# Kernel tuning notes

Hardware: AMD Instinct MI355X
Metric: run time of the kernel (lower is better)

The kernel has to match this reference:

```python
import jax, jax.numpy as jnp
import numpy as np

B, P, C = 128, 8732, 21          # batch, num_priors (SSD300), num_classes incl. background
TOP_K = 200
VAR0, VAR1 = 0.1, 0.2            # SSD prior variances
CONF_THRESH = 0.01
NMS_THRESH = 0.45


def setup_inputs() -> dict:
    key = jax.random.key(0)
    k1, k2, k3, k4 = jax.random.split(key, 4)
    loc_data = jax.random.normal(k1, (B, P, 4), jnp.float32)
    conf_data = jax.random.normal(k2, (B * P, C), jnp.float32)
    # priors: (cx, cy, w, h) in [0,1], positive widths/heights
    cxy = jax.random.uniform(k3, (P, 2), jnp.float32)
    wh = jax.random.uniform(k4, (P, 2), jnp.float32, minval=0.02, maxval=0.3)
    prior_data = jnp.concatenate([cxy, wh], axis=-1)
    return {"loc_data": loc_data, "conf_data": conf_data, "prior_data": prior_data}


def _decode(loc, priors):
    # loc: [B,P,4], priors: [P,4] (cx,cy,w,h) -> corner boxes [B,P,4]
    xy = priors[:, :2] + loc[..., :2] * VAR0 * priors[:, 2:]
    wh = priors[:, 2:] * jnp.exp(loc[..., 2:] * VAR1)
    return jnp.concatenate([xy - wh * 0.5, xy + wh * 0.5], axis=-1)


def _nms_single(boxes, scores, idxs):
    # boxes [P,4] corners, scores [P] (-1 where below conf_thresh), idxs [P] int class ids
    x1, y1, x2, y2 = boxes[:, 0], boxes[:, 1], boxes[:, 2], boxes[:, 3]
    areas = (x2 - x1) * (y2 - y1)

    def body(s, _):
        i = jnp.argmax(s)          # highest remaining score
        si = s[i]
        valid = si > 0.0
        bi = boxes[i]
        # IoU of bi against all boxes
        ix1 = jnp.maximum(bi[0], x1)
        iy1 = jnp.maximum(bi[1], y1)
        ix2 = jnp.minimum(bi[2], x2)
        iy2 = jnp.minimum(bi[3], y2)
        inter = jnp.maximum(ix2 - ix1, 0.0) * jnp.maximum(iy2 - iy1, 0.0)
        area_i = (bi[2] - bi[0]) * (bi[3] - bi[1])
        iou = inter / (area_i + areas - inter)
        # class-aware (batched) NMS: only suppress same-class boxes; also kills i itself (iou=1)
        suppress = (iou > NMS_THRESH) & (idxs == idxs[i])
        s_new = jnp.where(suppress, -1.0, s)
        row = jnp.where(
            valid,
            jnp.concatenate([bi, si[None], idxs[i].astype(jnp.float32)[None]]),
            jnp.zeros(6, dtype=boxes.dtype),
        )
        return s_new, row

    _, rows = jax.lax.scan(body, scores, None, length=TOP_K)
    return rows  # [TOP_K, 6] = (x1,y1,x2,y2,score,class)


def reference(loc_data, conf_data, prior_data):
    # softmax over classes, drop background, per-prior best fg class
    conf = jax.nn.softmax(conf_data, axis=-1)[:, 1:].reshape(B, P, C - 1)
    scores = conf.max(axis=-1)           # [B,P]
    cls = jnp.argmax(conf, axis=-1)      # [B,P] fg class id (0..C-2)
    boxes = _decode(loc_data, prior_data)  # [B,P,4]
    masked = jnp.where(scores > CONF_THRESH, scores, -1.0)
    return jax.vmap(_nms_single)(boxes, masked, cls)  # [B, TOP_K, 6]
```

## Files before the change

### kernel.cpp

```cpp
#include <hip/hip_runtime.h>


typedef unsigned long long u64;

#define BATCH 128
#define NPRIOR 8732
#define NCLS 21
#define TOPK 200
#define T 1024
#define TARGET 256
#define CAP 384
#define NBIN 4096
#define KW 6
#define TILE 1024

__device__ __forceinline__ double exp_fast(double x) {
  const double LOG2E = 1.4426950408889634;
  const double LN2_HI = 6.93147180369123816490e-01;
  const double LN2_LO = 1.90821492927058770002e-10;
  double n = rint(x * LOG2E);
  double r = fma(-n, LN2_HI, x);
  r = fma(-n, LN2_LO, r);
  double p = 2.505210838544172e-08;
  p = fma(p, r, 2.755731922398589e-07);
  p = fma(p, r, 2.7557319223985893e-06);
  p = fma(p, r, 2.48015873015873e-05);
  p = fma(p, r, 1.984126984126984e-04);
  p = fma(p, r, 1.388888888888889e-03);
  p = fma(p, r, 8.333333333333333e-03);
  p = fma(p, r, 4.1666666666666664e-02);
  p = fma(p, r, 1.6666666666666666e-01);
  p = fma(p, r, 0.5);
  p = fma(p, r, 1.0);
  p = fma(p, r, 1.0);
  return ldexp(p, (int)n);
}

__device__ __forceinline__ void radix_cut(const int* hist, int tid, int tcap,
                                          int* wtot, int* cut) {
  if (tid == 0) cut[2] = 0;
  const int base = tid * 4;
  const int cs = hist[base] + hist[base + 1] + hist[base + 2] + hist[base + 3];
  const int lane = tid & 63;
  int suf = cs;
#pragma unroll
  for (int off = 1; off < 64; off <<= 1) {
    int v = __shfl_down(suf, off);
    if (lane + off < 64) suf += v;
  }
  if (lane == 0) wtot[tid >> 6] = suf;
  __syncthreads();
  if (tid < 16) {
    int v = wtot[tid];
    int s = v;
#pragma unroll
    for (int off = 1; off < 16; off <<= 1) {
      int o = __shfl_down(s, off);
      if (tid + off < 16) s += o;
    }
    if (tid == 0) wtot[16] = s;
    wtot[tid] = s - v;
  }
  __syncthreads();
  const int total = wtot[16];
  if (total > 0) {
    const int target = total < tcap ? total : tcap;
    const int S = suf + wtot[tid >> 6];
    const int Snext = S - cs;
    if (S >= target && Snext < target) {
      int acc = Snext;
      for (int bn = base + 3; bn >= base; --bn) {
        acc += hist[bn];
        if (acc >= target) {
          cut[0] = bn; cut[1] = acc - hist[bn]; cut[2] = acc;
          break;
        }
      }
    }
  }
  __syncthreads();
}

__global__ __launch_bounds__(T) void detect_fused(
    const float* __restrict__ loc, const float* __restrict__ conf,
    const float* __restrict__ prior, float* __restrict__ out) {
  __shared__ u64 Ks[NPRIOR];
  __shared__ __align__(16) char pool[86016];
  __shared__ int wtot[17];
  __shared__ int cut1[3], cut2[3];
  __shared__ u64 Ash[KW], KFsh[KW], ACCsh[KW];
  __shared__ float4 abox[TOPK];
  __shared__ float aar[TOPK];
  __shared__ int acl[TOPK];
  __shared__ int sh_cnt, sh_nA;
  __shared__ u64 sh_ub;

  const int tid = threadIdx.x;
  const int b = blockIdx.x;
  const float* confb = conf + (long long)b * (NPRIOR * NCLS);
  const float4* loc4 = ((const float4*)loc) + (long long)b * NPRIOR;
  const float4* pr4 = (const float4*)prior;
  float* outb = out + (long long)b * (TOPK * 6);

  if (tid == 0) { sh_nA = 0; sh_ub = ~0ULL; }

  {
    float* stage = (float*)pool;
    for (int tile = 0; tile < NPRIOR; tile += TILE) {
      const int rows = (NPRIOR - tile < TILE) ? (NPRIOR - tile) : TILE;
      const int nf4 = (rows * NCLS) >> 2;
      const float4* src = (const float4*)(confb + (long long)tile * NCLS);
      float4* dst = (float4*)stage;
      for (int k = tid; k < nf4; k += T) dst[k] = src[k];
      __syncthreads();
      if (tid < rows) {
        const float* row = stage + tid * NCLS;
        float m = row[0];
#pragma unroll
        for (int j = 1; j < NCLS; ++j) m = fmaxf(m, row[j]);
        float sum = __expf(row[0] - m);
        float bestr = row[1];
        float beste = __expf(row[1] - m);
        sum += beste;
        int bi = 1;
#pragma unroll
        for (int j = 2; j < NCLS; ++j) {
          float rv = row[j];
          float ej = __expf(rv - m);
          sum += ej;
          if (rv > bestr) { bestr = rv; bi = j; beste = ej; }
        }
        float score = __fdividef(beste, sum);
        const int p = tile + tid;
        u64 key = 0ULL;
        if (score > 0.01f) {
          key = ((u64)__float_as_uint(score) << 32) |
                ((u64)(16383 - p) << 10) | (u64)(bi - 1);
        }
        Ks[p] = key;
      }
      __syncthreads();
    }
  }

  int* hist = (int*)pool;
  u64* buf = (u64*)(pool + 16384);
  u64* ebuf = (u64*)(pool + 19456);
  u64* buf2 = (u64*)(pool + 22528);
  float4* cbox = (float4*)(pool + 25600);
  float* car = (float*)(pool + 31744);
  int* ccl = (int*)(pool + 33280);
  u64* KILL = (u64*)(pool + 34816);

  while (true) {
    for (int i = tid; i < NBIN; i += T) hist[i] = 0;
    __syncthreads();
    const u64 ub = sh_ub;
    for (int i = tid; i < NPRIOR; i += T) {
      u64 k = Ks[i];
      if (k && k < ub) atomicAdd(&hist[(int)((k >> 46) & 0xFFF)], 1);
    }
    __syncthreads();
    radix_cut(hist, tid, TARGET, wtot, cut1);
    const int total = wtot[16];
    int M = cut1[2];
    if (M == 0) break;
    const int c1 = cut1[0];
    const int baseA = cut1[1];
    const bool need2 = (M > CAP);
    int c2 = 0;
    if (need2) {
      for (int i = tid; i < NBIN; i += T) hist[i] = 0;
      __syncthreads();
      for (int i = tid; i < NPRIOR; i += T) {
        u64 k = Ks[i];
        if (k && k < ub && (int)((k >> 46) & 0xFFF) == c1)
          atomicAdd(&hist[(int)((k >> 34) & 0xFFF)], 1);
      }
      __syncthreads();
      const int tcap2 = (total < TARGET ? total : TARGET) - baseA;
      radix_cut(hist, tid, tcap2, wtot, cut2);
      c2 = cut2[0];
      M = baseA + cut2[2];
      if (M > CAP) {
        int Md = M - hist[c2];
        if (Md > 0) { M = Md; c2 = c2 + 1; } else { M = CAP; }
      }
    }
    if (tid == 0) {
      sh_cnt = 0;
      sh_ub = need2 ? (((u64)c1 << 46) + ((u64)c2 << 34)) : ((u64)c1 << 46);
    }
    __syncthreads();
    for (int i = tid; i < NPRIOR; i += T) {
      u64 k = Ks[i];
      bool psel = false;
      if (k && k < ub) {
        int b1 = (int)((k >> 46) & 0xFFF);
        psel = need2 ? (b1 > c1 || (b1 == c1 && (int)((k >> 34) & 0xFFF) >= c2))
                     : (b1 >= c1);
      }
      u64 mask = __ballot(psel ? 1 : 0);
      if (mask) {
        int lane = tid & 63;
        int leader = __ffsll((unsigned long long)mask) - 1;
        int bpos = 0;
        if (lane == leader) bpos = atomicAdd(&sh_cnt, __popcll(mask));
        bpos = __shfl(bpos, leader);
        if (psel) {
          int pos = bpos + __popcll(mask & ((1ULL << lane) - 1ULL));
          if (pos < CAP) buf[pos] = k;
        }
      }
    }
    __syncthreads();
    int Mr = sh_cnt;
    if (Mr > CAP) Mr = CAP;
    if (Mr == 0) break;
    if (tid < Mr) {
      u64 ak = buf[tid];
      int cl = (int)(ak & 0x1FULL);
      int p = 16383 - (int)((ak >> 10) & 0x3FFFULL);
      const float* crow = confb + (long long)p * NCLS;
      double m = (double)crow[0];
#pragma unroll
      for (int j = 1; j < NCLS; ++j) m = fmax(m, (double)crow[j]);
      double sum = 0.0, best = -1.0;
#pragma unroll
      for (int j = 0; j < NCLS; ++j) {
        double ej = exp_fast((double)crow[j] - m);
        sum += ej;
        if (j >= 1 && ej > best) best = ej;
      }
      double score = best / sum;
      u64 sb = (u64)__double_as_longlong(score);
      ebuf[tid] = ((sb >> 24) << 24) | ((u64)(16383 - p) << 10) | (u64)cl;
    }
    __syncthreads();
    if (tid < Mr) {
      u64 ka = ebuf[tid];
      int ra = 0;
      for (int i = 0; i < Mr; ++i) ra += (ebuf[i] > ka);
      buf2[ra] = ka;
    }
    if (tid < KW) { Ash[tid] = 0ULL; KFsh[tid] = 0ULL; }
    __syncthreads();
    const int nA0 = sh_nA;
    if (tid < Mr) {
      const int t = tid;
      u64 k = buf2[t];
      int cl = (int)(k & 0x1FULL);
      int p = 16383 - (int)((k >> 10) & 0x3FFFULL);
      float4 l = loc4[p];
      float4 pr = pr4[p];
      double cx = (double)pr.x + (double)l.x * 0.1 * (double)pr.z;
      double cy = (double)pr.y + (double)l.y * 0.1 * (double)pr.w;
      double w = (double)pr.z * exp_fast((double)l.z * 0.2);
      double h = (double)pr.w * exp_fast((double)l.w * 0.2);
      float x1 = (float)(cx - w * 0.5), y1 = (float)(cy - h * 0.5);
      float x2 = (float)(cx + w * 0.5), y2 = (float)(cy + h * 0.5);
      cbox[t] = make_float4(x1, y1, x2, y2);
      car[t] = (x2 - x1) * (y2 - y1);
      ccl[t] = cl;
    }
    __syncthreads();
    if (nA0 > 0 && tid < Mr) {
      const int t = tid;
      float4 my = cbox[t];
      float mar = car[t];
      int mcl = ccl[t];
      bool sup = false;
      for (int a = 0; a < nA0; ++a) {
        if (acl[a] == mcl) {
          float4 ab = abox[a];
          float ix1 = fmaxf(ab.x, my.x), iy1 = fmaxf(ab.y, my.y);
          float ix2 = fminf(ab.z, my.z), iy2 = fminf(ab.w, my.w);
          float inter = fmaxf(ix2 - ix1, 0.f) * fmaxf(iy2 - iy1, 0.f);
          if (inter > 0.45f * (aar[a] + mar - inter)) sup = true;
        }
      }
      if (sup) atomicOr(&Ash[t >> 6], 1ULL << (t & 63));
    }
    for (int idx = tid; idx < KW * 512; idx += T) {
      const int seg = idx >> 9;
      const int t = idx & 511;
      if (t < Mr) {
        const int i0 = seg * 64;
        int i1 = i0 + 64;
        if (i1 > Mr) i1 = Mr;
        u64 mm = 0ULL;
        if (i1 > t) {
          float4 my = cbox[t];
          float mar = car[t];
          int mcl = ccl[t];
          int is = (i0 > t + 1) ? i0 : (t + 1);
          for (int i = is; i < i1; ++i) {
            if (ccl[i] == mcl) {
              float4 cb = cbox[i];
              float ix1 = fmaxf(my.x, cb.x), iy1 = fmaxf(my.y, cb.y);
              float ix2 = fminf(my.z, cb.z), iy2 = fminf(my.w, cb.w);
              float inter = fmaxf(ix2 - ix1, 0.f) * fmaxf(iy2 - iy1, 0.f);
              if (inter > 0.45f * (mar + car[i] - inter))
                mm |= 1ULL << (i - i0);
            }
          }
        }
        KILL[t * KW + seg] = mm;
        if (mm) atomicOr(&KFsh[t >> 6], 1ULL << (t & 63));
      }
    }
    __syncthreads();
    if (tid < 64) {
      u64 A0, A1, A2, A3, A4, A5;
      {
        u64 v[KW];
#pragma unroll
        for (int w = 0; w < KW; ++w) {
          int rem = Mr - 64 * w;
          u64 vm = (rem >= 64) ? ~0ULL : (rem <= 0 ? 0ULL : ((1ULL << rem) - 1ULL));
          v[w] = vm & ~Ash[w];
        }
        A0 = v[0]; A1 = v[1]; A2 = v[2]; A3 = v[3]; A4 = v[4]; A5 = v[5];
      }
      u64 C0 = 0, C1 = 0, C2 = 0, C3 = 0, C4 = 0, C5 = 0;
      int nacc = nA0;
      bool full = false;
#define KILLUPD(cidx) do { const u64* kc = &KILL[(cidx) * KW];      \
      A0 &= ~kc[0]; A1 &= ~kc[1]; A2 &= ~kc[2];                     \
      A3 &= ~kc[3]; A4 &= ~kc[4]; A5 &= ~kc[5]; } while (0)
#define RESW(w, Aw, Cw) if (!full) {                                \
      const u64 KFw = KFsh[w];                                      \
      int lim = Mr - (w) * 64; if (lim > 64) lim = 64;              \
      for (int q = 0; q < lim; ++q) {                               \
        if ((Aw >> q) & 1ULL) {                                     \
          Cw |= 1ULL << q; ++nacc;                                  \
          if (nacc == TOPK) { full = true; break; }                 \
          if ((KFw >> q) & 1ULL) KILLUPD((w) * 64 + q);             \
        } } }
      RESW(0, A0, C0)
      RESW(1, A1, C1)
      RESW(2, A2, C2)
      RESW(3, A3, C3)
      RESW(4, A4, C4)
      RESW(5, A5, C5)
#undef RESW
#undef KILLUPD
      if (tid == 0) {
        ACCsh[0] = C0; ACCsh[1] = C1; ACCsh[2] = C2;
        ACCsh[3] = C3; ACCsh[4] = C4; ACCsh[5] = C5;
        sh_nA = nacc;
      }
    }
    __syncthreads();
    if (tid < Mr) {
      const int t = tid;
      const int w = t >> 6, q = t & 63;
      const u64 accw = ACCsh[w];
      if ((accw >> q) & 1ULL) {
        int rank = nA0;
#pragma unroll
        for (int w2 = 0; w2 < KW; ++w2)
          if (w2 < w) rank += __popcll(ACCsh[w2]);
        rank += __popcll(accw & ((q == 0) ? 0ULL : ((1ULL << q) - 1ULL)));
        float4 bx = cbox[t];
        float sc = (float)__longlong_as_double((long long)((buf2[t] >> 24) << 24));
        float* o = outb + rank * 6;
        o[0] = bx.x; o[1] = bx.y; o[2] = bx.z; o[3] = bx.w;
        o[4] = sc; o[5] = (float)ccl[t];
        abox[rank] = bx; aar[rank] = car[t]; acl[rank] = ccl[t];
      }
    }
    __syncthreads();
    if (sh_nA >= TOPK) break;
    if (total - Mr <= 0) break;
  }
  const int nAf = sh_nA;
  for (int i = nAf * 6 + tid; i < TOPK * 6; i += T) outb[i] = 0.0f;
}

extern "C" void kernel_launch(void* const* d_in, const int* in_sizes, int n_in,
                              void* d_out, int out_size, void* d_ws,
                              size_t ws_size, hipStream_t stream) {
  const float* loc = (const float*)d_in[0];
  const float* conf = (const float*)d_in[1];
  const float* prior = (const float*)d_in[2];
  float* out = (float*)d_out;
  detect_fused<<<BATCH, T, 0, stream>>>(loc, conf, prior, out);
}
```

Measured before the change: 223.5 us.

## Split softmax/key scoring into a separate wide-grid prep kernel before NMS

Moves the per-prior softmax, best-class selection and sort-key construction out of the 128-block fused kernel into its own kernel with about 4366 blocks of 256 threads. The keys are written to workspace, and the NMS kernel loads them into shared memory. The aim is to spread the bandwidth-heavy softmax over the whole GPU instead of only 128 CUs, and to shrink the NMS kernel's shared pool. In exchange it adds a second launch and a global round-trip for the keys. It also relies on B*P being divisible by 256, which holds here.

```diff
diff --git a/kernel.cpp b/kernel.cpp
--- a/kernel.cpp
+++ b/kernel.cpp
@@ -12,7 +12,6 @@
 #define CAP 384
 #define NBIN 4096
 #define KW 6
-#define TILE 1024
 
 __device__ __forceinline__ double exp_fast(double x) {
   const double LOG2E = 1.4426950408889634;
@@ -36,6 +35,44 @@
   return ldexp(p, (int)n);
 }
 
+__global__ __launch_bounds__(256) void prep_kernel(
+    const float* __restrict__ conf, u64* __restrict__ keys) {
+  __shared__ __align__(16) float srow[256 * NCLS];
+  const int tid = threadIdx.x;
+  const long long R0 = (long long)blockIdx.x * 256;
+  const float4* src = (const float4*)(conf + R0 * NCLS);
+  float4* dst = (float4*)srow;
+  for (int k = tid; k < 1344; k += 256) dst[k] = src[k];
+  __syncthreads();
+
+  const float* row = srow + tid * NCLS;
+  float m = row[0];
+#pragma unroll
+  for (int j = 1; j < NCLS; ++j) m = fmaxf(m, row[j]);
+  float sum = __expf(row[0] - m);
+  float bestr = row[1];
+  float beste = __expf(row[1] - m);
+  sum += beste;
+  int bi = 1;
+#pragma unroll
+  for (int j = 2; j < NCLS; ++j) {
+    float rv = row[j];
+    float ej = __expf(rv - m);
+    sum += ej;
+    if (rv > bestr) { bestr = rv; bi = j; beste = ej; }
+  }
+  float score = __fdividef(beste, sum);
+
+  const long long r = R0 + tid;
+  const int p = (int)(r % NPRIOR);
+  u64 key = 0ULL;
+  if (score > 0.01f) {
+    key = ((u64)__float_as_uint(score) << 32) |
+          ((u64)(16383 - p) << 10) | (u64)(bi - 1);
+  }
+  keys[r] = key;
+}
+
 __device__ __forceinline__ void radix_cut(const int* hist, int tid, int tcap,
                                           int* wtot, int* cut) {
   if (tid == 0) cut[2] = 0;
@@ -81,11 +118,12 @@
   __syncthreads();
 }
 
-__global__ __launch_bounds__(T) void detect_fused(
+__global__ __launch_bounds__(T) void nms_kernel(
     const float* __restrict__ loc, const float* __restrict__ conf,
-    const float* __restrict__ prior, float* __restrict__ out) {
+    const float* __restrict__ prior, const u64* __restrict__ keys,
+    float* __restrict__ out) {
   __shared__ u64 Ks[NPRIOR];
-  __shared__ __align__(16) char pool[86016];
+  __shared__ __align__(16) char pool[53248];
   __shared__ int wtot[17];
   __shared__ int cut1[3], cut2[3];
   __shared__ u64 Ash[KW], KFsh[KW], ACCsh[KW];
@@ -102,46 +140,9 @@
   const float4* pr4 = (const float4*)prior;
   float* outb = out + (long long)b * (TOPK * 6);
 
+  for (int i = tid; i < NPRIOR; i += T) Ks[i] = keys[(long long)b * NPRIOR + i];
   if (tid == 0) { sh_nA = 0; sh_ub = ~0ULL; }
-
-  {
-    float* stage = (float*)pool;
-    for (int tile = 0; tile < NPRIOR; tile += TILE) {
-      const int rows = (NPRIOR - tile < TILE) ? (NPRIOR - tile) : TILE;
-      const int nf4 = (rows * NCLS) >> 2;
-      const float4* src = (const float4*)(confb + (long long)tile * NCLS);
-      float4* dst = (float4*)stage;
-      for (int k = tid; k < nf4; k += T) dst[k] = src[k];
-      __syncthreads();
-      if (tid < rows) {
-        const float* row = stage + tid * NCLS;
-        float m = row[0];
-#pragma unroll
-        for (int j = 1; j < NCLS; ++j) m = fmaxf(m, row[j]);
-        float sum = __expf(row[0] - m);
-        float bestr = row[1];
-        float beste = __expf(row[1] - m);
-        sum += beste;
-        int bi = 1;
-#pragma unroll
-        for (int j = 2; j < NCLS; ++j) {
-          float rv = row[j];
-          float ej = __expf(rv - m);
-          sum += ej;
-          if (rv > bestr) { bestr = rv; bi = j; beste = ej; }
-        }
-        float score = __fdividef(beste, sum);
-        const int p = tile + tid;
-        u64 key = 0ULL;
-        if (score > 0.01f) {
-          key = ((u64)__float_as_uint(score) << 32) |
-                ((u64)(16383 - p) << 10) | (u64)(bi - 1);
-        }
-        Ks[p] = key;
-      }
-      __syncthreads();
-    }
-  }
+  __syncthreads();
 
   int* hist = (int*)pool;
   u64* buf = (u64*)(pool + 16384);
@@ -385,5 +386,10 @@
   const float* conf = (const float*)d_in[1];
   const float* prior = (const float*)d_in[2];
   float* out = (float*)d_out;
-  detect_fused<<<BATCH, T, 0, stream>>>(loc, conf, prior, out);
-}
+
+  u64* keys = (u64*)d_ws;
+
+  const int nrows_blocks = (BATCH * NPRIOR) / 256;
+  prep_kernel<<<nrows_blocks, 256, 0, stream>>>(conf, keys);
+  nms_kernel<<<BATCH, T, 0, stream>>>(loc, conf, prior, keys, out);
+}
```

New measurement: 211.2 us. 5.5% less time.
